# Kernel optimization log

Measured on AMD Instinct MI355X. Metric: run time of the kernel, lower is better.

## Reference

```python
import jax, jax.numpy as jnp
import numpy as np
import math

B, S, D, H = 4, 2048, 768, 12
HD = D // H  # 64


def setup_inputs() -> dict:
    key = jax.random.key(0)
    ks = jax.random.split(key, 9)
    s = 0.02
    return {
        "hidden_states": jax.random.normal(ks[0], (B, S, D), jnp.float32),
        "layout_q": jax.random.normal(ks[1], (B, S, D), jnp.float32),
        "layout_k": jax.random.normal(ks[2], (B, S, D), jnp.float32),
        "attention_mask": jnp.zeros((B, 1, 1, S), jnp.float32),
        "Wq": jax.random.normal(ks[3], (D, D), jnp.float32) * s,
        "bq": jnp.zeros((D,), jnp.float32),
        "Wk": jax.random.normal(ks[4], (D, D), jnp.float32) * s,
        "bk": jnp.zeros((D,), jnp.float32),
        "Wv": jax.random.normal(ks[5], (D, D), jnp.float32) * s,
        "bv": jnp.zeros((D,), jnp.float32),
    }


def _split_heads(x):
    # [B,S,D] -> [B,H,S,HD]
    return x.reshape(B, S, H, HD).transpose(0, 2, 1, 3)


def reference(hidden_states, layout_q, layout_k, attention_mask, Wq, bq, Wk, bk, Wv, bv):
    q = _split_heads(hidden_states @ Wq.T + bq)
    k = _split_heads(hidden_states @ Wk.T + bk)
    v = _split_heads(hidden_states @ Wv.T + bv)
    lq = _split_heads(layout_q)
    lk = _split_heads(layout_k)
    scale = 1.0 / math.sqrt(HD)
    # dual-stream scores: content + layout, both [B,H,S,S]
    scores = (jnp.einsum("bhqd,bhkd->bhqk", q, k)
              + jnp.einsum("bhqd,bhkd->bhqk", lq, lk)) * scale
    scores = scores + attention_mask
    probs = jax.nn.softmax(scores, axis=-1)
    ctx = jnp.einsum("bhqk,bhkd->bhqd", probs, v)
    return ctx.transpose(0, 2, 1, 3).reshape(B, S, D)
```

## Files before the change

kernel.cpp:

```cpp
#include <hip/hip_runtime.h>


typedef __attribute__((ext_vector_type(8))) short short8;
typedef __attribute__((ext_vector_type(4))) float floatx4;

#define LOG2E 1.4426950408889634f
#define QSCL 0.18033688011112042f

static constexpr int Sn = 2048, Dn = 768, Hn = 12, BHn = 48;

__device__ __forceinline__ unsigned short f2bf(float f) {
  unsigned u = __float_as_uint(f);
  u += 0x7FFFu + ((u >> 16) & 1u);
  return (unsigned short)(u >> 16);
}

typedef const __attribute__((address_space(1))) unsigned int* gas_t;
typedef __attribute__((address_space(3))) unsigned int* las_t;
__device__ __forceinline__ void async16(const void* g, void* l) {
  __builtin_amdgcn_global_load_lds((gas_t)g, (las_t)l, 16, 0, 0);
}

__global__ void cast_hs_kernel(const float* __restrict__ in, unsigned short* __restrict__ out, int n4) {
  int i = blockIdx.x * 256 + threadIdx.x;
  if (i >= n4) return;
  float4 v = ((const float4*)in)[i];
  ushort4 o = make_ushort4(f2bf(v.x), f2bf(v.y), f2bf(v.z), f2bf(v.w));
  ((ushort4*)out)[i] = o;
}

__global__ void cast_w_kernel(const float* __restrict__ w0, const float* __restrict__ w1,
                              const float* __restrict__ w2, unsigned short* __restrict__ out) {
  int i = blockIdx.x * 256 + threadIdx.x;
  const float* src = (blockIdx.y == 0) ? w0 : (blockIdx.y == 1) ? w1 : w2;
  float4 v = ((const float4*)src)[i];
  ushort4 o = make_ushort4(f2bf(v.x), f2bf(v.y), f2bf(v.z), f2bf(v.w));
  ((ushort4*)(out + (size_t)blockIdx.y * Dn * Dn))[i] = o;
}

__global__ void pack_layout_kernel(const float* __restrict__ lq, const float* __restrict__ lk,
                                   unsigned short* __restrict__ Qc, unsigned short* __restrict__ Kc) {
  int idx = blockIdx.x * 256 + threadIdx.x;
  const float* src = blockIdx.y ? lk : lq;
  unsigned short* dst = blockIdx.y ? Kc : Qc;
  const float sc = blockIdx.y ? 1.0f : QSCL;
  int d8 = idx & 7;
  int tt = idx >> 3;
  int h = tt % Hn;
  int bs = tt / Hn;
  int b = bs >> 11, s = bs & (Sn - 1);
  float4 v0 = ((const float4*)src)[idx * 2];
  float4 v1 = ((const float4*)src)[idx * 2 + 1];
  short8 o;
  o[0] = (short)f2bf(v0.x * sc); o[1] = (short)f2bf(v0.y * sc);
  o[2] = (short)f2bf(v0.z * sc); o[3] = (short)f2bf(v0.w * sc);
  o[4] = (short)f2bf(v1.x * sc); o[5] = (short)f2bf(v1.y * sc);
  o[6] = (short)f2bf(v1.z * sc); o[7] = (short)f2bf(v1.w * sc);
  size_t off = ((size_t)(b * Hn + h) * Sn + s) * 128 + 64 + d8 * 8;
  *(short8*)(dst + off) = o;
}

__global__ __launch_bounds__(256, 3)
void proj_kernel(const unsigned short* __restrict__ X,
                 const unsigned short* __restrict__ Wb,
                 const float* __restrict__ bq, const float* __restrict__ bk, const float* __restrict__ bv,
                 unsigned short* __restrict__ Qc, unsigned short* __restrict__ Kc,
                 unsigned short* __restrict__ Vt) {
  __shared__ __align__(16) unsigned short sMem[16384];

  const int z = blockIdx.z;
  const unsigned short* W = Wb + (size_t)z * Dn * Dn;
  const float* bias = (z == 0) ? bq : (z == 1) ? bk : bv;

  const int t = threadIdx.x;
  const int lane = t & 63, wave = t >> 6;
  const int wm = wave >> 1, wn = wave & 1;
  const int quad = lane >> 4, col15 = lane & 15;
  const int m0 = blockIdx.y * 128, n0 = blockIdx.x * 128;

  const int srow = lane >> 2, schunk = lane & 3;

  floatx4 acc[4][4];
#pragma unroll
  for (int i = 0; i < 4; i++)
#pragma unroll
    for (int j = 0; j < 4; j++) acc[i][j] = (floatx4){0.f, 0.f, 0.f, 0.f};

  auto stageAB = [&](int kt, int buf) {
    unsigned short* sA = sMem + buf * 4096;
    unsigned short* sB = sMem + 8192 + buf * 4096;
#pragma unroll
    for (int c = 0; c < 2; c++) {
      int row = wave * 32 + c * 16 + srow;
      async16(X + (size_t)(m0 + row) * Dn + kt * 32 + schunk * 8, sA + (wave * 32 + c * 16) * 32);
      async16(W + (size_t)(n0 + row) * Dn + kt * 32 + schunk * 8, sB + (wave * 32 + c * 16) * 32);
    }
  };

  stageAB(0, 0);
  __syncthreads();

  for (int kt = 0; kt < 24; kt++) {
    const int cur = kt & 1;
    if (kt + 1 < 24) stageAB(kt + 1, cur ^ 1);
    const unsigned short* sA = sMem + cur * 4096;
    const unsigned short* sB = sMem + 8192 + cur * 4096;
    short8 af[4], bf[4];
#pragma unroll
    for (int i = 0; i < 4; i++)
      af[i] = *(const short8*)(sA + (wm * 64 + i * 16 + col15) * 32 + quad * 8);
#pragma unroll
    for (int j = 0; j < 4; j++)
      bf[j] = *(const short8*)(sB + (wn * 64 + j * 16 + col15) * 32 + quad * 8);
#pragma unroll
    for (int i = 0; i < 4; i++)
#pragma unroll
      for (int j = 0; j < 4; j++)
        acc[i][j] = __builtin_amdgcn_mfma_f32_16x16x32_bf16(af[i], bf[j], acc[i][j], 0, 0, 0);
    __syncthreads();
  }

  const int b = m0 >> 11;
  const int s0g = m0 & (Sn - 1);
  const int h0 = n0 >> 6;

  if (z < 2) {
    const float scl = (z == 0) ? QSCL : 1.0f;
    unsigned short* dst0 = (z == 0) ? Qc : Kc;
#pragma unroll
    for (int j = 0; j < 4; j++) {
      int nl = wn * 64 + j * 16 + col15;
      float bias_n = bias[n0 + nl];
#pragma unroll
      for (int i = 0; i < 4; i++) {
        int mb = wm * 64 + i * 16 + quad * 4;
#pragma unroll
        for (int r = 0; r < 4; r++) {
          int m = mb + r;
          sMem[m * 128 + (nl ^ (((m >> 2) & 3) << 4))] = f2bf((acc[i][j][r] + bias_n) * scl);
        }
      }
    }
    __syncthreads();
#pragma unroll
    for (int cc = 0; cc < 8; cc++) {
      int idx = cc * 256 + t;
      int m = idx >> 4, piece = idx & 15;
      int h = h0 + (piece >> 3), d8 = piece & 7;
      short8 v = *(const short8*)(sMem + m * 128 + (piece ^ (((m >> 2) & 3) << 1)) * 8);
      *(short8*)(dst0 + ((size_t)(b * Hn + h) * Sn + s0g + m) * 128 + d8 * 8) = v;
    }
  } else {
#pragma unroll
    for (int j = 0; j < 4; j++) {
      int nl = wn * 64 + j * 16 + col15;
      float bias_n = bias[n0 + nl];
#pragma unroll
      for (int i = 0; i < 4; i++) {
        int mb = wm * 64 + i * 16 + quad * 4;
        ushort4 pk = make_ushort4(f2bf(acc[i][j][0] + bias_n), f2bf(acc[i][j][1] + bias_n),
                                  f2bf(acc[i][j][2] + bias_n), f2bf(acc[i][j][3] + bias_n));
        *(ushort4*)(sMem + nl * 128 + (mb ^ ((nl & 7) << 4))) = pk;
      }
    }
    __syncthreads();
#pragma unroll
    for (int cc = 0; cc < 8; cc++) {
      int idx = cc * 256 + t;
      int nl = idx >> 4, piece = idx & 15;
      int h = h0 + (nl >> 6), d = nl & 63;
      short8 v = *(const short8*)(sMem + nl * 128 + (piece ^ ((nl & 7) << 1)) * 8);
      *(short8*)(Vt + ((size_t)(b * Hn + h) * 64 + d) * Sn + s0g + piece * 8) = v;
    }
  }
}

__global__ __launch_bounds__(256, 3)
void attn_kernel(const unsigned short* __restrict__ Qc,
                 const unsigned short* __restrict__ Kc,
                 const unsigned short* __restrict__ Vt,
                 const float* __restrict__ mask,
                 float* __restrict__ out) {
  __shared__ __align__(16) unsigned short sK[64 * 128];
  __shared__ __align__(16) unsigned short sV2[2][64 * 64];
  __shared__ __align__(16) unsigned short sS[128 * 64];

  const int t = threadIdx.x;
  const int lane = t & 63, wave = t >> 6;
  const int quad = lane >> 4, col15 = lane & 15;
  const int swz = (col15 & 7) << 3;

  const int id = blockIdx.x;
  const int slot = id >> 3;
  const int bh = (id & 7) + 8 * (slot >> 4);
  const int q0 = (slot & 15) * 128;
  const int b = bh / Hn, h = bh % Hn;

  short8 aq[2][4];
  const unsigned short* Qbase = Qc + ((size_t)bh * Sn + q0) * 128;
#pragma unroll
  for (int i = 0; i < 2; i++)
#pragma unroll
    for (int kk = 0; kk < 4; kk++)
      aq[i][kk] = *(const short8*)(Qbase + (size_t)(wave * 32 + i * 16 + col15) * 128 + kk * 32 + quad * 8);

  floatx4 O[2][4];
  float lsum[2] = {0.f, 0.f};
#pragma unroll
  for (int i = 0; i < 2; i++)
#pragma unroll
    for (int j = 0; j < 4; j++) O[i][j] = (floatx4){0.f, 0.f, 0.f, 0.f};

  const unsigned short* Kbase = Kc + (size_t)bh * Sn * 128;
  const unsigned short* Vbase = Vt + (size_t)bh * 64 * Sn;
  const float* mbase = mask + (size_t)b * Sn;

  const int krow = lane >> 4, kslot = lane & 15;
  const int vrow = lane >> 3, vslot = lane & 7;

  auto stageK = [&](int tile) {
#pragma unroll
    for (int c = 0; c < 4; c++) {
      int row = wave * 16 + c * 4 + krow;
      int g = (kslot & 8) | ((kslot ^ row) & 7);
      async16(Kbase + (size_t)(tile * 64 + row) * 128 + g * 8, sK + (wave * 16 + c * 4) * 128);
    }
  };
  auto stageV = [&](int tile, int buf) {
    unsigned short* sVn = &sV2[buf][0];
#pragma unroll
    for (int c = 0; c < 2; c++) {
      int row = wave * 16 + c * 8 + vrow;
      int g = vslot ^ (row & 7);
      async16(Vbase + (size_t)row * Sn + tile * 64 + g * 8, sVn + (wave * 16 + c * 8) * 64);
    }
  };

  constexpr int NT = Sn / 64;
  stageK(0);
  stageV(0, 0);
  float mcur = mbase[lane] * LOG2E;
  __syncthreads();

  for (int kt = 0; kt < NT; kt++) {
    const int cur = kt & 1;
    const unsigned short* sVcur = &sV2[cur][0];

    floatx4 sacc[4][2];
#pragma unroll
    for (int jm = 0; jm < 4; jm++) {
      sacc[jm][0] = (floatx4){0.f, 0.f, 0.f, 0.f};
      sacc[jm][1] = (floatx4){0.f, 0.f, 0.f, 0.f};
    }
    __builtin_amdgcn_s_setprio(1);
#pragma unroll
    for (int kk = 0; kk < 4; kk++) {
      const int slotK = (((kk * 4 + quad) & 8) | (((kk * 4 + quad) ^ col15) & 7)) * 8;
#pragma unroll
      for (int jm = 0; jm < 4; jm++) {
        short8 ak = *(const short8*)(sK + (jm * 16 + col15) * 128 + slotK);
        sacc[jm][0] = __builtin_amdgcn_mfma_f32_16x16x32_bf16(ak, aq[0][kk], sacc[jm][0], 0, 0, 0);
        sacc[jm][1] = __builtin_amdgcn_mfma_f32_16x16x32_bf16(ak, aq[1][kk], sacc[jm][1], 0, 0, 0);
      }
    }
    __builtin_amdgcn_s_setprio(0);

    const int tn = (kt + 1 < NT) ? kt + 1 : NT - 1;
    float mnew = mbase[tn * 64 + lane] * LOG2E;
    const bool nomask = __all(mcur == 0.0f);

    __syncthreads();
    if (kt + 1 < NT) {
      stageK(kt + 1);
      stageV(kt + 1, cur ^ 1);
    }

    float mvv[4][4];
    if (!nomask) {
#pragma unroll
      for (int jm = 0; jm < 4; jm++)
#pragma unroll
        for (int r = 0; r < 4; r++) mvv[jm][r] = __shfl(mcur, jm * 16 + quad * 4 + r);
    }

#pragma unroll
    for (int iq = 0; iq < 2; iq++) {
      unsigned short* srow = sS + (wave * 32 + iq * 16 + col15) * 64;
      float lacc = 0.f;
#pragma unroll
      for (int jm = 0; jm < 4; jm++) {
        float p0 = sacc[jm][iq][0], p1 = sacc[jm][iq][1];
        float p2 = sacc[jm][iq][2], p3 = sacc[jm][iq][3];
        if (!nomask) { p0 += mvv[jm][0]; p1 += mvv[jm][1]; p2 += mvv[jm][2]; p3 += mvv[jm][3]; }
        unsigned u0 = __float_as_uint(__builtin_amdgcn_exp2f(p0)) & 0xFFFF0000u;
        unsigned u1 = __float_as_uint(__builtin_amdgcn_exp2f(p1)) & 0xFFFF0000u;
        unsigned u2 = __float_as_uint(__builtin_amdgcn_exp2f(p2)) & 0xFFFF0000u;
        unsigned u3 = __float_as_uint(__builtin_amdgcn_exp2f(p3)) & 0xFFFF0000u;
        lacc += (__uint_as_float(u0) + __uint_as_float(u1)) +
                (__uint_as_float(u2) + __uint_as_float(u3));
        uint2 w;
        w.x = (u0 >> 16) | u1;
        w.y = (u2 >> 16) | u3;
        *(uint2*)(srow + ((jm * 16 + quad * 4) ^ swz)) = w;
      }
      lsum[iq] += lacc;
    }

    __builtin_amdgcn_s_setprio(1);
#pragma unroll
    for (int kk = 0; kk < 2; kk++) {
      short8 pb0 = *(const short8*)(sS + (wave * 32 + col15) * 64 + ((kk * 32 + quad * 8) ^ swz));
      short8 pb1 = *(const short8*)(sS + (wave * 32 + 16 + col15) * 64 + ((kk * 32 + quad * 8) ^ swz));
      const int slotV = ((kk * 4 + quad) ^ (col15 & 7)) * 8;
#pragma unroll
      for (int jd = 0; jd < 4; jd++) {
        short8 av = *(const short8*)(sVcur + (jd * 16 + col15) * 64 + slotV);
        O[0][jd] = __builtin_amdgcn_mfma_f32_16x16x32_bf16(av, pb0, O[0][jd], 0, 0, 0);
        O[1][jd] = __builtin_amdgcn_mfma_f32_16x16x32_bf16(av, pb1, O[1][jd], 0, 0, 0);
      }
    }
    __builtin_amdgcn_s_setprio(0);

    __syncthreads();
    mcur = mnew;
  }

#pragma unroll
  for (int iq = 0; iq < 2; iq++) {
    float s_ = lsum[iq];
    s_ += __shfl_xor(s_, 16);
    s_ += __shfl_xor(s_, 32);
    float inv = 1.0f / s_;
    int qrow = q0 + wave * 32 + iq * 16 + col15;
    float* obase = out + ((size_t)b * Sn + qrow) * Dn + h * 64 + quad * 4;
#pragma unroll
    for (int jd = 0; jd < 4; jd++) {
      float4 o4 = make_float4(O[iq][jd][0] * inv, O[iq][jd][1] * inv,
                              O[iq][jd][2] * inv, O[iq][jd][3] * inv);
      *(float4*)(obase + jd * 16) = o4;
    }
  }
}

extern "C" void kernel_launch(void* const* d_in, const int* in_sizes, int n_in,
                              void* d_out, int out_size, void* d_ws, size_t ws_size,
                              hipStream_t stream) {
  const float* hs   = (const float*)d_in[0];
  const float* lq   = (const float*)d_in[1];
  const float* lk   = (const float*)d_in[2];
  const float* mask = (const float*)d_in[3];
  const float* Wq   = (const float*)d_in[4];
  const float* bq   = (const float*)d_in[5];
  const float* Wk   = (const float*)d_in[6];
  const float* bk   = (const float*)d_in[7];
  const float* Wv   = (const float*)d_in[8];
  const float* bv   = (const float*)d_in[9];
  float* out = (float*)d_out;

  char* ws = (char*)d_ws;
  unsigned short* Xbf = (unsigned short*)ws;
  unsigned short* Wbf = (unsigned short*)(ws + 12582912);
  unsigned short* Qc  = (unsigned short*)(ws + 12582912 + 3538944);
  unsigned short* Kc  = Qc + (size_t)BHn * Sn * 128;
  unsigned short* Vt  = Kc + (size_t)BHn * Sn * 128;

  cast_hs_kernel<<<6144, 256, 0, stream>>>(hs, Xbf, 1572864);
  cast_w_kernel<<<dim3(576, 3), 256, 0, stream>>>(Wq, Wk, Wv, Wbf);
  pack_layout_kernel<<<dim3(3072, 2), 256, 0, stream>>>(lq, lk, Qc, Kc);
  proj_kernel<<<dim3(6, 64, 3), 256, 0, stream>>>(Xbf, Wbf, bq, bk, bv, Qc, Kc, Vt);
  attn_kernel<<<768, 256, 0, stream>>>(Qc, Kc, Vt, mask, out);
}
```

Baseline: 274.9 us.

## Split attention block into 8 waves of 16 query rows each

```diff
diff --git a/kernel.cpp b/kernel.cpp
--- a/kernel.cpp
+++ b/kernel.cpp
@@ -175,7 +175,7 @@
   }
 }
 
-__global__ __launch_bounds__(256, 3)
+__global__ __launch_bounds__(512, 6)
 void attn_kernel(const unsigned short* __restrict__ Qc,
                  const unsigned short* __restrict__ Kc,
                  const unsigned short* __restrict__ Vt,
@@ -196,20 +196,16 @@
   const int q0 = (slot & 15) * 128;
   const int b = bh / Hn, h = bh % Hn;
 
-  short8 aq[2][4];
+  short8 aq[4];
   const unsigned short* Qbase = Qc + ((size_t)bh * Sn + q0) * 128;
 #pragma unroll
-  for (int i = 0; i < 2; i++)
-#pragma unroll
-    for (int kk = 0; kk < 4; kk++)
-      aq[i][kk] = *(const short8*)(Qbase + (size_t)(wave * 32 + i * 16 + col15) * 128 + kk * 32 + quad * 8);
-
-  floatx4 O[2][4];
-  float lsum[2] = {0.f, 0.f};
-#pragma unroll
-  for (int i = 0; i < 2; i++)
-#pragma unroll
-    for (int j = 0; j < 4; j++) O[i][j] = (floatx4){0.f, 0.f, 0.f, 0.f};
+  for (int kk = 0; kk < 4; kk++)
+    aq[kk] = *(const short8*)(Qbase + (size_t)(wave * 16 + col15) * 128 + kk * 32 + quad * 8);
+
+  floatx4 O[4];
+  float lsum = 0.f;
+#pragma unroll
+  for (int j = 0; j < 4; j++) O[j] = (floatx4){0.f, 0.f, 0.f, 0.f};
 
   const unsigned short* Kbase = Kc + (size_t)bh * Sn * 128;
   const unsigned short* Vbase = Vt + (size_t)bh * 64 * Sn;
@@ -220,19 +216,18 @@
 
   auto stageK = [&](int tile) {
 #pragma unroll
-    for (int c = 0; c < 4; c++) {
-      int row = wave * 16 + c * 4 + krow;
+    for (int c = 0; c < 2; c++) {
+      int row = wave * 8 + c * 4 + krow;
       int g = (kslot & 8) | ((kslot ^ row) & 7);
-      async16(Kbase + (size_t)(tile * 64 + row) * 128 + g * 8, sK + (wave * 16 + c * 4) * 128);
+      async16(Kbase + (size_t)(tile * 64 + row) * 128 + g * 8, sK + (wave * 8 + c * 4) * 128);
     }
   };
   auto stageV = [&](int tile, int buf) {
     unsigned short* sVn = &sV2[buf][0];
-#pragma unroll
-    for (int c = 0; c < 2; c++) {
-      int row = wave * 16 + c * 8 + vrow;
+    {
+      int row = wave * 8 + vrow;
       int g = vslot ^ (row & 7);
-      async16(Vbase + (size_t)row * Sn + tile * 64 + g * 8, sVn + (wave * 16 + c * 8) * 64);
+      async16(Vbase + (size_t)row * Sn + tile * 64 + g * 8, sVn + (wave * 8) * 64);
     }
   };
 
@@ -246,12 +241,9 @@
     const int cur = kt & 1;
     const unsigned short* sVcur = &sV2[cur][0];
 
-    floatx4 sacc[4][2];
-#pragma unroll
-    for (int jm = 0; jm < 4; jm++) {
-      sacc[jm][0] = (floatx4){0.f, 0.f, 0.f, 0.f};
-      sacc[jm][1] = (floatx4){0.f, 0.f, 0.f, 0.f};
-    }
+    floatx4 sacc[4];
+#pragma unroll
+    for (int jm = 0; jm < 4; jm++) sacc[jm] = (floatx4){0.f, 0.f, 0.f, 0.f};
     __builtin_amdgcn_s_setprio(1);
 #pragma unroll
     for (int kk = 0; kk < 4; kk++) {
@@ -259,8 +251,7 @@
 #pragma unroll
       for (int jm = 0; jm < 4; jm++) {
         short8 ak = *(const short8*)(sK + (jm * 16 + col15) * 128 + slotK);
-        sacc[jm][0] = __builtin_amdgcn_mfma_f32_16x16x32_bf16(ak, aq[0][kk], sacc[jm][0], 0, 0, 0);
-        sacc[jm][1] = __builtin_amdgcn_mfma_f32_16x16x32_bf16(ak, aq[1][kk], sacc[jm][1], 0, 0, 0);
+        sacc[jm] = __builtin_amdgcn_mfma_f32_16x16x32_bf16(ak, aq[kk], sacc[jm], 0, 0, 0);
       }
     }
     __builtin_amdgcn_s_setprio(0);
@@ -283,14 +274,13 @@
         for (int r = 0; r < 4; r++) mvv[jm][r] = __shfl(mcur, jm * 16 + quad * 4 + r);
     }
 
-#pragma unroll
-    for (int iq = 0; iq < 2; iq++) {
-      unsigned short* srow = sS + (wave * 32 + iq * 16 + col15) * 64;
+    {
+      unsigned short* srow = sS + (wave * 16 + col15) * 64;
       float lacc = 0.f;
 #pragma unroll
       for (int jm = 0; jm < 4; jm++) {
-        float p0 = sacc[jm][iq][0], p1 = sacc[jm][iq][1];
-        float p2 = sacc[jm][iq][2], p3 = sacc[jm][iq][3];
+        float p0 = sacc[jm][0], p1 = sacc[jm][1];
+        float p2 = sacc[jm][2], p3 = sacc[jm][3];
         if (!nomask) { p0 += mvv[jm][0]; p1 += mvv[jm][1]; p2 += mvv[jm][2]; p3 += mvv[jm][3]; }
         unsigned u0 = __float_as_uint(__builtin_amdgcn_exp2f(p0)) & 0xFFFF0000u;
         unsigned u1 = __float_as_uint(__builtin_amdgcn_exp2f(p1)) & 0xFFFF0000u;
@@ -303,20 +293,18 @@
         w.y = (u2 >> 16) | u3;
         *(uint2*)(srow + ((jm * 16 + quad * 4) ^ swz)) = w;
       }
-      lsum[iq] += lacc;
+      lsum += lacc;
     }
 
     __builtin_amdgcn_s_setprio(1);
 #pragma unroll
     for (int kk = 0; kk < 2; kk++) {
-      short8 pb0 = *(const short8*)(sS + (wave * 32 + col15) * 64 + ((kk * 32 + quad * 8) ^ swz));
-      short8 pb1 = *(const short8*)(sS + (wave * 32 + 16 + col15) * 64 + ((kk * 32 + quad * 8) ^ swz));
+      short8 pb = *(const short8*)(sS + (wave * 16 + col15) * 64 + ((kk * 32 + quad * 8) ^ swz));
       const int slotV = ((kk * 4 + quad) ^ (col15 & 7)) * 8;
 #pragma unroll
       for (int jd = 0; jd < 4; jd++) {
         short8 av = *(const short8*)(sVcur + (jd * 16 + col15) * 64 + slotV);
-        O[0][jd] = __builtin_amdgcn_mfma_f32_16x16x32_bf16(av, pb0, O[0][jd], 0, 0, 0);
-        O[1][jd] = __builtin_amdgcn_mfma_f32_16x16x32_bf16(av, pb1, O[1][jd], 0, 0, 0);
+        O[jd] = __builtin_amdgcn_mfma_f32_16x16x32_bf16(av, pb, O[jd], 0, 0, 0);
       }
     }
     __builtin_amdgcn_s_setprio(0);
@@ -325,18 +313,17 @@
     mcur = mnew;
   }
 
-#pragma unroll
-  for (int iq = 0; iq < 2; iq++) {
-    float s_ = lsum[iq];
+  {
+    float s_ = lsum;
     s_ += __shfl_xor(s_, 16);
     s_ += __shfl_xor(s_, 32);
     float inv = 1.0f / s_;
-    int qrow = q0 + wave * 32 + iq * 16 + col15;
+    int qrow = q0 + wave * 16 + col15;
     float* obase = out + ((size_t)b * Sn + qrow) * Dn + h * 64 + quad * 4;
 #pragma unroll
     for (int jd = 0; jd < 4; jd++) {
-      float4 o4 = make_float4(O[iq][jd][0] * inv, O[iq][jd][1] * inv,
-                              O[iq][jd][2] * inv, O[iq][jd][3] * inv);
+      float4 o4 = make_float4(O[jd][0] * inv, O[jd][1] * inv,
+                              O[jd][2] * inv, O[jd][3] * inv);
       *(float4*)(obase + jd * 16) = o4;
     }
   }
@@ -368,5 +355,5 @@
   cast_w_kernel<<<dim3(576, 3), 256, 0, stream>>>(Wq, Wk, Wv, Wbf);
   pack_layout_kernel<<<dim3(3072, 2), 256, 0, stream>>>(lq, lk, Qc, Kc);
   proj_kernel<<<dim3(6, 64, 3), 256, 0, stream>>>(Xbf, Wbf, bq, bk, bv, Qc, Kc, Vt);
-  attn_kernel<<<768, 256, 0, stream>>>(Qc, Kc, Vt, mask, out);
-}
+  attn_kernel<<<768, 512, 0, stream>>>(Qc, Kc, Vt, mask, out);
+}
```

Measured after the change: 356.7 us. 29.8% more time.

## Give each attention wave 64 query rows using two waves per block

Applied to the files above, without the earlier changes.

```diff
diff --git a/kernel.cpp b/kernel.cpp
--- a/kernel.cpp
+++ b/kernel.cpp
@@ -175,7 +175,7 @@
   }
 }
 
-__global__ __launch_bounds__(256, 3)
+__global__ __launch_bounds__(128, 3)
 void attn_kernel(const unsigned short* __restrict__ Qc,
                  const unsigned short* __restrict__ Kc,
                  const unsigned short* __restrict__ Vt,
@@ -196,20 +196,20 @@
   const int q0 = (slot & 15) * 128;
   const int b = bh / Hn, h = bh % Hn;
 
-  short8 aq[2][4];
+  short8 aq[4][4];
   const unsigned short* Qbase = Qc + ((size_t)bh * Sn + q0) * 128;
 #pragma unroll
-  for (int i = 0; i < 2; i++)
+  for (int iq = 0; iq < 4; iq++)
 #pragma unroll
     for (int kk = 0; kk < 4; kk++)
-      aq[i][kk] = *(const short8*)(Qbase + (size_t)(wave * 32 + i * 16 + col15) * 128 + kk * 32 + quad * 8);
-
-  floatx4 O[2][4];
-  float lsum[2] = {0.f, 0.f};
-#pragma unroll
-  for (int i = 0; i < 2; i++)
-#pragma unroll
-    for (int j = 0; j < 4; j++) O[i][j] = (floatx4){0.f, 0.f, 0.f, 0.f};
+      aq[iq][kk] = *(const short8*)(Qbase + (size_t)(wave * 64 + iq * 16 + col15) * 128 + kk * 32 + quad * 8);
+
+  floatx4 O[4][4];
+  float lsum[4] = {0.f, 0.f, 0.f, 0.f};
+#pragma unroll
+  for (int iq = 0; iq < 4; iq++)
+#pragma unroll
+    for (int j = 0; j < 4; j++) O[iq][j] = (floatx4){0.f, 0.f, 0.f, 0.f};
 
   const unsigned short* Kbase = Kc + (size_t)bh * Sn * 128;
   const unsigned short* Vbase = Vt + (size_t)bh * 64 * Sn;
@@ -220,19 +220,19 @@
 
   auto stageK = [&](int tile) {
 #pragma unroll
-    for (int c = 0; c < 4; c++) {
-      int row = wave * 16 + c * 4 + krow;
+    for (int c = 0; c < 8; c++) {
+      int row = wave * 32 + c * 4 + krow;
       int g = (kslot & 8) | ((kslot ^ row) & 7);
-      async16(Kbase + (size_t)(tile * 64 + row) * 128 + g * 8, sK + (wave * 16 + c * 4) * 128);
+      async16(Kbase + (size_t)(tile * 64 + row) * 128 + g * 8, sK + (wave * 32 + c * 4) * 128);
     }
   };
   auto stageV = [&](int tile, int buf) {
     unsigned short* sVn = &sV2[buf][0];
 #pragma unroll
-    for (int c = 0; c < 2; c++) {
-      int row = wave * 16 + c * 8 + vrow;
+    for (int c = 0; c < 4; c++) {
+      int row = wave * 32 + c * 8 + vrow;
       int g = vslot ^ (row & 7);
-      async16(Vbase + (size_t)row * Sn + tile * 64 + g * 8, sVn + (wave * 16 + c * 8) * 64);
+      async16(Vbase + (size_t)row * Sn + tile * 64 + g * 8, sVn + (wave * 32 + c * 8) * 64);
     }
   };
 
@@ -246,12 +246,11 @@
     const int cur = kt & 1;
     const unsigned short* sVcur = &sV2[cur][0];
 
-    floatx4 sacc[4][2];
-#pragma unroll
-    for (int jm = 0; jm < 4; jm++) {
-      sacc[jm][0] = (floatx4){0.f, 0.f, 0.f, 0.f};
-      sacc[jm][1] = (floatx4){0.f, 0.f, 0.f, 0.f};
-    }
+    floatx4 sacc[4][4];
+#pragma unroll
+    for (int jm = 0; jm < 4; jm++)
+#pragma unroll
+      for (int iq = 0; iq < 4; iq++) sacc[jm][iq] = (floatx4){0.f, 0.f, 0.f, 0.f};
     __builtin_amdgcn_s_setprio(1);
 #pragma unroll
     for (int kk = 0; kk < 4; kk++) {
@@ -259,8 +258,9 @@
 #pragma unroll
       for (int jm = 0; jm < 4; jm++) {
         short8 ak = *(const short8*)(sK + (jm * 16 + col15) * 128 + slotK);
-        sacc[jm][0] = __builtin_amdgcn_mfma_f32_16x16x32_bf16(ak, aq[0][kk], sacc[jm][0], 0, 0, 0);
-        sacc[jm][1] = __builtin_amdgcn_mfma_f32_16x16x32_bf16(ak, aq[1][kk], sacc[jm][1], 0, 0, 0);
+#pragma unroll
+        for (int iq = 0; iq < 4; iq++)
+          sacc[jm][iq] = __builtin_amdgcn_mfma_f32_16x16x32_bf16(ak, aq[iq][kk], sacc[jm][iq], 0, 0, 0);
       }
     }
     __builtin_amdgcn_s_setprio(0);
@@ -284,8 +284,8 @@
     }
 
 #pragma unroll
-    for (int iq = 0; iq < 2; iq++) {
-      unsigned short* srow = sS + (wave * 32 + iq * 16 + col15) * 64;
+    for (int iq = 0; iq < 4; iq++) {
+      unsigned short* srow = sS + (wave * 64 + iq * 16 + col15) * 64;
       float lacc = 0.f;
 #pragma unroll
       for (int jm = 0; jm < 4; jm++) {
@@ -309,14 +309,17 @@
     __builtin_amdgcn_s_setprio(1);
 #pragma unroll
     for (int kk = 0; kk < 2; kk++) {
-      short8 pb0 = *(const short8*)(sS + (wave * 32 + col15) * 64 + ((kk * 32 + quad * 8) ^ swz));
-      short8 pb1 = *(const short8*)(sS + (wave * 32 + 16 + col15) * 64 + ((kk * 32 + quad * 8) ^ swz));
+      short8 pb[4];
+#pragma unroll
+      for (int iq = 0; iq < 4; iq++)
+        pb[iq] = *(const short8*)(sS + (wave * 64 + iq * 16 + col15) * 64 + ((kk * 32 + quad * 8) ^ swz));
       const int slotV = ((kk * 4 + quad) ^ (col15 & 7)) * 8;
 #pragma unroll
       for (int jd = 0; jd < 4; jd++) {
         short8 av = *(const short8*)(sVcur + (jd * 16 + col15) * 64 + slotV);
-        O[0][jd] = __builtin_amdgcn_mfma_f32_16x16x32_bf16(av, pb0, O[0][jd], 0, 0, 0);
-        O[1][jd] = __builtin_amdgcn_mfma_f32_16x16x32_bf16(av, pb1, O[1][jd], 0, 0, 0);
+#pragma unroll
+        for (int iq = 0; iq < 4; iq++)
+          O[iq][jd] = __builtin_amdgcn_mfma_f32_16x16x32_bf16(av, pb[iq], O[iq][jd], 0, 0, 0);
       }
     }
     __builtin_amdgcn_s_setprio(0);
@@ -326,12 +329,12 @@
   }
 
 #pragma unroll
-  for (int iq = 0; iq < 2; iq++) {
+  for (int iq = 0; iq < 4; iq++) {
     float s_ = lsum[iq];
     s_ += __shfl_xor(s_, 16);
     s_ += __shfl_xor(s_, 32);
     float inv = 1.0f / s_;
-    int qrow = q0 + wave * 32 + iq * 16 + col15;
+    int qrow = q0 + wave * 64 + iq * 16 + col15;
     float* obase = out + ((size_t)b * Sn + qrow) * Dn + h * 64 + quad * 4;
 #pragma unroll
     for (int jd = 0; jd < 4; jd++) {
@@ -368,5 +371,5 @@
   cast_w_kernel<<<dim3(576, 3), 256, 0, stream>>>(Wq, Wk, Wv, Wbf);
   pack_layout_kernel<<<dim3(3072, 2), 256, 0, stream>>>(lq, lk, Qc, Kc);
   proj_kernel<<<dim3(6, 64, 3), 256, 0, stream>>>(Xbf, Wbf, bq, bk, bv, Qc, Kc, Vt);
-  attn_kernel<<<768, 256, 0, stream>>>(Qc, Kc, Vt, mask, out);
-}
+  attn_kernel<<<768, 128, 0, stream>>>(Qc, Kc, Vt, mask, out);
+}
```

Result: slower. 345.5 us (+25.7%).
